# Kernel tuning notes

Hardware: AMD Instinct MI355X
Metric: run time of the kernel (lower is better)

Reference implementation:

```python
import jax, jax.numpy as jnp
import numpy as np

B, S, D, H = 2, 2048, 1024, 16
DK = D // H
SCALE = DK ** 0.5


def setup_inputs() -> dict:
    key = jax.random.key(0)
    ks = jax.random.split(key, 5)
    std = 1.0 / np.sqrt(D)
    return {
        "x": jax.random.normal(ks[0], (B, S, D), dtype=jnp.float32),
        "Wq": jax.random.normal(ks[1], (D, D), dtype=jnp.float32) * std,
        "Wk": jax.random.normal(ks[2], (D, D), dtype=jnp.float32) * std,
        "Wv": jax.random.normal(ks[3], (D, D), dtype=jnp.float32) * std,
        "Wo": jax.random.normal(ks[4], (D, D), dtype=jnp.float32) * std,
    }


def _split_heads(t):
    # [B, S, D] -> [B, H, S, DK]
    b, s, d = t.shape
    return t.reshape(b, s, H, DK).transpose(0, 2, 1, 3)


def reference(x, Wq, Wk, Wv, Wo):
    b, s, d = x.shape
    q = _split_heads(x @ Wq)
    k = _split_heads(x @ Wk)
    v = _split_heads(x @ Wv)
    # scores: [B, H, S, S]
    score = jnp.einsum("bhqd,bhkd->bhqk", q, k)
    causal = jnp.tril(jnp.ones((s, s), dtype=bool))[None, None]
    score = jnp.where(causal, score, -jnp.inf)
    attn = jax.nn.softmax(score / SCALE, axis=-1)
    out = jnp.einsum("bhqk,bhkd->bhqd", attn, v)
    out = out.transpose(0, 2, 1, 3).reshape(b, s, d)
    return out @ Wo
```

## Files before the change

### kernel.cpp

```cpp
#include <hip/hip_runtime.h>
#include <hip/hip_bf16.h>

typedef __bf16 bf16;
typedef __bf16 bf16x4 __attribute__((ext_vector_type(4)));
typedef __bf16 bf16x8 __attribute__((ext_vector_type(8)));
typedef float f32x4 __attribute__((ext_vector_type(4)));

#define MFMA16(a, b, c) __builtin_amdgcn_mfma_f32_16x16x32_bf16((a), (b), (c), 0, 0, 0)

__device__ __forceinline__ void async16(const void* g, void* l) {
  typedef const unsigned int __attribute__((address_space(1))) * GP;
  typedef unsigned int __attribute__((address_space(3))) * LP;
  __builtin_amdgcn_global_load_lds((GP)g, (LP)l, 16, 0, 0);
}

__global__ __launch_bounds__(256) void prep(
    const float* __restrict__ w0, const float* __restrict__ w1,
    const float* __restrict__ w2, const float* __restrict__ w3,
    const float* __restrict__ x, bf16* __restrict__ wtOut,
    bf16* __restrict__ xOut) {
  const int t = threadIdx.x;
  if (blockIdx.z == 4) {
    size_t base = ((size_t)(blockIdx.y * 16 + blockIdx.x)) * 16384;
#pragma unroll
    for (int p = 0; p < 16; ++p) {
      size_t i = base + (size_t)(p * 256 + t) * 4;
      f32x4 v = *(const f32x4*)&x[i];
      bf16 o[4];
#pragma unroll
      for (int j = 0; j < 4; ++j) o[j] = (bf16)v[j];
      *(ulong1*)&xOut[i] = *(ulong1*)o;
    }
    return;
  }
  __shared__ __align__(16) float tile[64][68];
  const float* src = (blockIdx.z == 0) ? w0 : (blockIdx.z == 1) ? w1
                   : (blockIdx.z == 2) ? w2 : w3;
  bf16* dst = wtOut + (size_t)blockIdx.z * (1024u * 1024u);
  const int bx = blockIdx.x, by = blockIdx.y;
#pragma unroll
  for (int p = 0; p < 4; ++p) {
    int idx = t + p * 256;
    int r = idx >> 4, c4 = idx & 15;
    *(f32x4*)&tile[r][c4 * 4] =
        *(const f32x4*)&src[(size_t)(by * 64 + r) * 1024 + bx * 64 + c4 * 4];
  }
  __syncthreads();
#pragma unroll
  for (int p = 0; p < 2; ++p) {
    int idx = t + p * 256;
    int rn = idx >> 3, c8 = idx & 7;
    bf16x8 v;
#pragma unroll
    for (int i = 0; i < 8; ++i) v[i] = (bf16)tile[c8 * 8 + i][rn];
    *(bf16x8*)&dst[(size_t)(bx * 64 + rn) * 1024 + by * 64 + c8 * 8] = v;
  }
}

template <typename OutT, int NI>
__global__ __launch_bounds__(256, 4) void gemm_bt(
    const bf16* __restrict__ A, const bf16* __restrict__ Bt,
    OutT* __restrict__ C, int btStrideZ, int cStrideZ, float scaleZ0,
    bf16* __restrict__ vtOut) {
  constexpr int XT = 1024 / (NI * 32);
  const int bid = blockIdx.x;
  const int rr = bid & 7, tt = bid >> 3;
  const int xb = tt % XT, yb = (tt / XT) * 8 + rr;
  const int zi = blockIdx.y;

  const int tid = threadIdx.x;
  const int wave = tid >> 6, lane = tid & 63;
  const int quad = lane >> 4, l16 = lane & 15;
  const int wm = wave >> 1, wn = wave & 1;
  const int m0 = yb * 128, n0 = xb * (NI * 32);
  const bf16* Bz = Bt + (size_t)zi * (size_t)btStrideZ;
  OutT* Cz = C + (size_t)zi * (size_t)cStrideZ;
  const float sc = (zi == 0) ? scaleZ0 : 1.0f;

  __shared__ __align__(16) bf16 lsA[2][128 * 32];
  __shared__ __align__(16) bf16 lsB[2][NI * 32 * 32];

  const int lrow = lane >> 2;
  const int cgX = (lane & 3) ^ ((lrow >> 1) & 3);
  const int fR = (l16 >> 1) & 3;

  f32x4 acc[4][NI];
#pragma unroll
  for (int i = 0; i < 4; ++i)
#pragma unroll
    for (int j = 0; j < NI; ++j) acc[i][j] = (f32x4){0.f, 0.f, 0.f, 0.f};

#pragma unroll
  for (int c = 0; c < 2; ++c) {
    int chunk = wave * 2 + c;
    int row = chunk * 16 + lrow;
    async16(&A[(size_t)(m0 + row) * 1024 + cgX * 8], &lsA[0][chunk * 512]);
  }
#pragma unroll
  for (int c = 0; c < NI / 2; ++c) {
    int chunk = wave * (NI / 2) + c;
    int row = chunk * 16 + lrow;
    async16(&Bz[(size_t)(n0 + row) * 1024 + cgX * 8], &lsB[0][chunk * 512]);
  }
  __syncthreads();

  for (int it = 0; it < 32; ++it) {
    const int cur = it & 1;
    if (it < 31) {
      int k0n = (it + 1) * 32;
#pragma unroll
      for (int c = 0; c < 2; ++c) {
        int chunk = wave * 2 + c;
        int row = chunk * 16 + lrow;
        async16(&A[(size_t)(m0 + row) * 1024 + k0n + cgX * 8],
                &lsA[cur ^ 1][chunk * 512]);
      }
#pragma unroll
      for (int c = 0; c < NI / 2; ++c) {
        int chunk = wave * (NI / 2) + c;
        int row = chunk * 16 + lrow;
        async16(&Bz[(size_t)(n0 + row) * 1024 + k0n + cgX * 8],
                &lsB[cur ^ 1][chunk * 512]);
      }
    }

    bf16x8 af[4], bfr[NI];
#pragma unroll
    for (int i = 0; i < 4; ++i) {
      int ra = wm * 64 + i * 16 + l16;
      af[i] = *(const bf16x8*)&lsA[cur][ra * 32 + ((quad ^ fR) * 8)];
    }
#pragma unroll
    for (int ni = 0; ni < NI; ++ni) {
      int rb = wn * (NI * 16) + ni * 16 + l16;
      bfr[ni] = *(const bf16x8*)&lsB[cur][rb * 32 + ((quad ^ fR) * 8)];
    }
#pragma unroll
    for (int mi = 0; mi < 4; ++mi)
#pragma unroll
      for (int ni = 0; ni < NI; ++ni)
        acc[mi][ni] = MFMA16(af[mi], bfr[ni], acc[mi][ni]);

    __syncthreads();
  }

  if (zi == 2 && vtOut != nullptr) {
#pragma unroll
    for (int mi = 0; mi < 4; ++mi)
#pragma unroll
      for (int ni = 0; ni < NI; ++ni) {
        int col = n0 + wn * (NI * 16) + ni * 16 + l16;
        int hd = col >> 6, d = col & 63;
        int row = m0 + wm * 64 + mi * 16 + quad * 4;
        int b = row >> 11, s = row & 2047;
        int s32 = s & 31;
        int sp = (s & ~31) + ((s32 & 12) << 1) + ((s32 >> 4) << 2);
        bf16 o[4];
#pragma unroll
        for (int r = 0; r < 4; ++r) o[r] = (bf16)acc[mi][ni][r];
        *(ulong1*)&vtOut[((size_t)(b * 16 + hd) * 64 + d) * 2048 + sp] =
            *(ulong1*)o;
      }
  } else {
#pragma unroll
    for (int mi = 0; mi < 4; ++mi)
#pragma unroll
      for (int ni = 0; ni < NI; ++ni) {
        int col = n0 + wn * (NI * 16) + ni * 16 + l16;
#pragma unroll
        for (int r = 0; r < 4; ++r) {
          int row = m0 + wm * 64 + mi * 16 + quad * 4 + r;
          Cz[(size_t)row * 1024 + col] = (OutT)(acc[mi][ni][r] * sc);
        }
      }
  }
}

__global__ __launch_bounds__(512, 4) void attn_fwd(
    const bf16* __restrict__ Q, const bf16* __restrict__ K,
    const bf16* __restrict__ Vt, bf16* __restrict__ O) {
  const int bid = blockIdx.x;
  const int x = bid & 15, hb = bid >> 4;
  const int h = hb & 15, b = hb >> 4;
  const int qt = b ? (15 - x) : x;
  const int tid = threadIdx.x;
  const int wave = tid >> 6, lane = tid & 63;
  const int quad = lane >> 4, l16 = lane & 15;
  const int wq = wave >> 1;
  const int par = wave & 1;

  __shared__ __align__(16) bf16 SMEM[32768];
  bf16* Qs = &SMEM[16384];

  const size_t base = ((size_t)b * 2048) * 1024 + (size_t)h * 64;
  const bf16* Qb = Q + base;
  const bf16* Kb = K + base;
  const bf16* Vtb = Vt + ((size_t)(b * 16 + h)) * 64 * 2048;
  bf16* Ob = O + base;

  const int lrow = lane >> 3;
  const int cgX = (lane & 7) ^ lrow;

#pragma unroll
  for (int c = 0; c < 2; ++c) {
    int chunk = wave * 2 + c;
    int row = chunk * 8 + lrow;
    async16(&Qb[(size_t)(qt * 128 + row) * 1024 + cgX * 8], &Qs[chunk * 512]);
  }
  {
    int row = wave * 8 + lrow;
    async16(&Kb[(size_t)row * 1024 + cgX * 8], &SMEM[0 * 8192 + wave * 512]);
    async16(&Vtb[(size_t)row * 2048 + cgX * 8],
            &SMEM[0 * 8192 + 4096 + wave * 512]);
    async16(&Kb[(size_t)(64 + row) * 1024 + cgX * 8],
            &SMEM[1 * 8192 + wave * 512]);
    async16(&Vtb[(size_t)row * 2048 + 64 + cgX * 8],
            &SMEM[1 * 8192 + 4096 + wave * 512]);
  }
  __syncthreads();

  bf16x8 aq[2][2];
#pragma unroll
  for (int g = 0; g < 2; ++g)
#pragma unroll
    for (int ks = 0; ks < 2; ++ks) {
      int row = wq * 32 + g * 16 + l16;
      aq[g][ks] =
          *(const bf16x8*)&Qs[row * 64 + (((ks * 4 + quad) ^ (l16 & 7)) * 8)];
    }
  __syncthreads();

  const float NEG_INF = -__builtin_inff();
  f32x4 lsv[2];
  f32x4 Oacc[2][4];
#pragma unroll
  for (int g = 0; g < 2; ++g) {
    lsv[g] = (f32x4){0.f, 0.f, 0.f, 0.f};
#pragma unroll
    for (int nt = 0; nt < 4; ++nt) Oacc[g][nt] = (f32x4){0.f, 0.f, 0.f, 0.f};
  }

  const int two_qt = 2 * qt;
  const int kt_end = 2 * qt + 1;

  for (int ktp = 0; ktp <= two_qt; ktp += 2) {
    {
      int row = wave * 8 + lrow;
      if (ktp + 2 <= kt_end) {
        int s2 = (ktp + 2) & 3;
        async16(&Kb[(size_t)((ktp + 2) * 64 + row) * 1024 + cgX * 8],
                &SMEM[s2 * 8192 + wave * 512]);
        async16(&Vtb[(size_t)row * 2048 + (ktp + 2) * 64 + cgX * 8],
                &SMEM[s2 * 8192 + 4096 + wave * 512]);
      }
      if (ktp + 3 <= kt_end) {
        int s3 = (ktp + 3) & 3;
        async16(&Kb[(size_t)((ktp + 3) * 64 + row) * 1024 + cgX * 8],
                &SMEM[s3 * 8192 + wave * 512]);
        async16(&Vtb[(size_t)row * 2048 + (ktp + 3) * 64 + cgX * 8],
                &SMEM[s3 * 8192 + 4096 + wave * 512]);
      }
    }

    const int kt = ktp + par;
    const int ko = (kt & 3) * 8192;
    const int vo = ko + 4096;
    const bool diag = (ktp == two_qt);
    const bool active = !diag || (par == 0) || (wq >= 2);

    if (active) {
#pragma unroll
      for (int a = 0; a < 2; ++a) {
        f32x4 s[2][2];
#pragma unroll
        for (int t = 0; t < 2; ++t) {
          const int nt = 2 * a + t;
          const int row = nt * 16 + l16;
          bf16x8 bk0 =
              *(const bf16x8*)&SMEM[ko + row * 64 + ((quad ^ (l16 & 7)) * 8)];
          bf16x8 bk1 = *(const bf16x8*)&SMEM[ko + row * 64 +
                                             (((4 + quad) ^ (l16 & 7)) * 8)];
#pragma unroll
          for (int g = 0; g < 2; ++g) {
            f32x4 sv = (f32x4){0.f, 0.f, 0.f, 0.f};
            sv = MFMA16(bk0, aq[g][0], sv);
            sv = MFMA16(bk1, aq[g][1], sv);
            s[g][t] = sv;
          }
        }

        if (diag) {
#pragma unroll
          for (int g = 0; g < 2; ++g) {
            const int q_rel = wq * 32 + g * 16 + l16;
#pragma unroll
            for (int t = 0; t < 2; ++t) {
              const int kb = par * 64 + (2 * a + t) * 16 + quad * 4;
#pragma unroll
              for (int r = 0; r < 4; ++r)
                if (kb + r > q_rel) s[g][t][r] = NEG_INF;
            }
          }
        }

        bf16x8 apf[2];
#pragma unroll
        for (int g = 0; g < 2; ++g) {
#pragma unroll
          for (int t = 0; t < 2; ++t) {
#pragma unroll
            for (int r = 0; r < 4; ++r) s[g][t][r] = exp2f(s[g][t][r]);
            lsv[g] += s[g][t];
          }
          bf16x4 c0 = __builtin_convertvector(s[g][0], bf16x4);
          bf16x4 c1 = __builtin_convertvector(s[g][1], bf16x4);
#pragma unroll
          for (int i = 0; i < 4; ++i) {
            apf[g][i] = c0[i];
            apf[g][4 + i] = c1[i];
          }
        }

#pragma unroll
        for (int nt = 0; nt < 4; ++nt) {
          const int R = nt * 16 + l16;
          bf16x8 bvf = *(const bf16x8*)&SMEM[vo + R * 64 +
                                             (((a * 4 + quad) ^ (l16 & 7)) *
                                              8)];
#pragma unroll
          for (int g = 0; g < 2; ++g)
            Oacc[g][nt] = MFMA16(apf[g], bvf, Oacc[g][nt]);
        }
      }
    }

    __syncthreads();
  }

  float ls[2];
#pragma unroll
  for (int g = 0; g < 2; ++g) {
    float a_ = lsv[g][0] + lsv[g][1] + lsv[g][2] + lsv[g][3];
    a_ += __shfl_xor(a_, 16, 64);
    a_ += __shfl_xor(a_, 32, 64);
    ls[g] = a_;
  }

  float* F = (float*)SMEM;
  const int roff = wq * 2176;
  if (par == 1) {
#pragma unroll
    for (int g = 0; g < 2; ++g) {
#pragma unroll
      for (int nt = 0; nt < 4; ++nt)
        *(f32x4*)&F[roff + (g * 4 + nt) * 256 + lane * 4] = Oacc[g][nt];
      F[roff + 2048 + g * 64 + lane] = ls[g];
    }
  }
  __syncthreads();
  if (par == 0) {
#pragma unroll
    for (int g = 0; g < 2; ++g) {
#pragma unroll
      for (int nt = 0; nt < 4; ++nt)
        Oacc[g][nt] += *(const f32x4*)&F[roff + (g * 4 + nt) * 256 + lane * 4];
      ls[g] += F[roff + 2048 + g * 64 + lane];
    }
    float rl[2][4];
#pragma unroll
    for (int g = 0; g < 2; ++g)
#pragma unroll
      for (int r = 0; r < 4; ++r)
        rl[g][r] = 1.f / __shfl(ls[g], quad * 4 + r, 64);
#pragma unroll
    for (int g = 0; g < 2; ++g)
#pragma unroll
      for (int nt = 0; nt < 4; ++nt)
#pragma unroll
        for (int r = 0; r < 4; ++r) {
          int row = qt * 128 + wq * 32 + g * 16 + quad * 4 + r;
          Ob[(size_t)row * 1024 + nt * 16 + l16] =
              (bf16)(Oacc[g][nt][r] * rl[g][r]);
        }
  }
}

extern "C" void kernel_launch(void* const* d_in, const int* in_sizes, int n_in,
                              void* d_out, int out_size, void* d_ws,
                              size_t ws_size, hipStream_t stream) {
  (void)in_sizes; (void)n_in; (void)out_size; (void)ws_size;
  const float* x  = (const float*)d_in[0];
  const float* Wq = (const float*)d_in[1];
  const float* Wk = (const float*)d_in[2];
  const float* Wv = (const float*)d_in[3];
  const float* Wo = (const float*)d_in[4];
  float* out = (float*)d_out;

  bf16* ws = (bf16*)d_ws;
  const size_t WELEM = 1024u * 1024u;
  const size_t TELEM = 4096u * 1024u;
  bf16* wt  = ws;
  bf16* xbf = ws + 4 * WELEM;
  bf16* q   = xbf + TELEM;
  bf16* k   = q + TELEM;
  bf16* vt  = k + TELEM;
  bf16* ao  = vt + TELEM;

  const float QSCALE = 0.125f * 1.44269504088896340736f;

  prep<<<dim3(16, 16, 5), 256, 0, stream>>>(Wq, Wk, Wv, Wo, x, wt, xbf);
  gemm_bt<bf16, 4><<<dim3(256, 3), 256, 0, stream>>>(
      xbf, wt, q, (int)WELEM, (int)TELEM, QSCALE, vt);
  attn_fwd<<<dim3(512), 512, 0, stream>>>(q, k, vt, ao);
  gemm_bt<float, 2><<<dim3(512, 1), 256, 0, stream>>>(
      ao, wt + 3 * WELEM, out, 0, 0, 1.0f, nullptr);
}
```

Measured before the change: 169.6 us.

## Add 256x256-tile QKV projection GEMM kernel with 512 threads

Replaces the generic QKV projection GEMM with a dedicated kernel using 256x256 output tiles, 8 waves, double-buffered async global-to-LDS loads with XOR swizzle, and setprio around the MFMA bursts. Larger tiles raise arithmetic intensity and cut redundant global loads of A and B. In exchange the grid shrinks to 192 blocks on a 256-CU device, and the 128 KB of LDS plus 128 accumulator floats per lane may limit occupancy. The output stores are scalar bf16 writes instead of vectorized ones.

Result: slower. 173.1 us (+2.1%).

```diff
diff --git a/kernel.cpp b/kernel.cpp
--- a/kernel.cpp
+++ b/kernel.cpp
@@ -54,6 +54,132 @@
 #pragma unroll
     for (int i = 0; i < 8; ++i) v[i] = (bf16)tile[c8 * 8 + i][rn];
     *(bf16x8*)&dst[(size_t)(bx * 64 + rn) * 1024 + by * 64 + c8 * 8] = v;
+  }
+}
+
+__global__ __launch_bounds__(512, 2) void qkv256(
+    const bf16* __restrict__ A, const bf16* __restrict__ Bt,
+    bf16* __restrict__ C, int btStrideZ, int cStrideZ, float scaleZ0,
+    bf16* __restrict__ vtOut) {
+  const int bid = blockIdx.x;
+  const int rr = bid & 7, tt = bid >> 3;
+  const int xb = tt & 3, yb = (tt >> 2) * 8 + rr;
+  const int zi = blockIdx.y;
+
+  const int tid = threadIdx.x;
+  const int wave = tid >> 6, lane = tid & 63;
+  const int quad = lane >> 4, l16 = lane & 15;
+  const int wm = wave >> 2, wn = wave & 3;
+  const int m0 = yb * 256, n0 = xb * 256;
+  const bf16* Bz = Bt + (size_t)zi * (size_t)btStrideZ;
+  bf16* Cz = C + (size_t)zi * (size_t)cStrideZ;
+  const float sc = (zi == 0) ? scaleZ0 : 1.0f;
+
+  __shared__ __align__(16) bf16 lsA[2][256 * 64];
+  __shared__ __align__(16) bf16 lsB[2][256 * 64];
+
+  const int lrow = lane >> 3;
+  const int cgX = (lane & 7) ^ lrow;
+
+  f32x4 acc[8][4];
+#pragma unroll
+  for (int i = 0; i < 8; ++i)
+#pragma unroll
+    for (int j = 0; j < 4; ++j) acc[i][j] = (f32x4){0.f, 0.f, 0.f, 0.f};
+
+#define QKV_STAGE(buf, kt)                                                   \
+  {                                                                          \
+    const int k0_ = (kt)*64;                                                 \
+    _Pragma("unroll") for (int c = 0; c < 4; ++c) {                          \
+      int chunk = wave * 4 + c;                                              \
+      int row = chunk * 8 + lrow;                                            \
+      async16(&A[(size_t)(m0 + row) * 1024 + k0_ + cgX * 8],                 \
+              &lsA[buf][chunk * 512]);                                       \
+    }                                                                        \
+    _Pragma("unroll") for (int c = 0; c < 4; ++c) {                          \
+      int chunk = wave * 4 + c;                                              \
+      int row = chunk * 8 + lrow;                                            \
+      async16(&Bz[(size_t)(n0 + row) * 1024 + k0_ + cgX * 8],                \
+              &lsB[buf][chunk * 512]);                                       \
+    }                                                                        \
+  }
+
+  QKV_STAGE(0, 0);
+  QKV_STAGE(1, 1);
+  asm volatile("s_waitcnt vmcnt(8)" ::: "memory");
+  __builtin_amdgcn_s_barrier();
+
+  for (int kt = 0; kt < 16; ++kt) {
+    const int cur = kt & 1;
+#pragma unroll
+    for (int ks = 0; ks < 2; ++ks) {
+      bf16x8 bfr[4];
+#pragma unroll
+      for (int ni = 0; ni < 4; ++ni) {
+        int rb = wn * 64 + ni * 16 + l16;
+        bfr[ni] = *(const bf16x8*)&lsB[cur][rb * 64 +
+                                            (((ks * 4 + quad) ^ (l16 & 7)) *
+                                             8)];
+      }
+#pragma unroll
+      for (int mh = 0; mh < 2; ++mh) {
+        bf16x8 af[4];
+#pragma unroll
+        for (int i = 0; i < 4; ++i) {
+          int ra = wm * 128 + (mh * 4 + i) * 16 + l16;
+          af[i] = *(const bf16x8*)&lsA[cur][ra * 64 +
+                                            (((ks * 4 + quad) ^ (l16 & 7)) *
+                                             8)];
+        }
+        __builtin_amdgcn_s_setprio(1);
+#pragma unroll
+        for (int i = 0; i < 4; ++i)
+#pragma unroll
+          for (int ni = 0; ni < 4; ++ni)
+            acc[mh * 4 + i][ni] = MFMA16(af[i], bfr[ni], acc[mh * 4 + i][ni]);
+        __builtin_amdgcn_s_setprio(0);
+      }
+    }
+    __builtin_amdgcn_s_barrier();
+    if (kt + 2 < 16) {
+      QKV_STAGE(cur, kt + 2);
+      asm volatile("s_waitcnt vmcnt(8)" ::: "memory");
+    } else {
+      asm volatile("s_waitcnt vmcnt(0)" ::: "memory");
+    }
+    __builtin_amdgcn_s_barrier();
+  }
+#undef QKV_STAGE
+
+  if (zi == 2 && vtOut != nullptr) {
+#pragma unroll
+    for (int mi = 0; mi < 8; ++mi)
+#pragma unroll
+      for (int ni = 0; ni < 4; ++ni) {
+        int col = n0 + wn * 64 + ni * 16 + l16;
+        int hd = col >> 6, d = col & 63;
+        int row = m0 + wm * 128 + mi * 16 + quad * 4;
+        int b = row >> 11, s = row & 2047;
+        int s32 = s & 31;
+        int sp = (s & ~31) + ((s32 & 12) << 1) + ((s32 >> 4) << 2);
+        bf16 o[4];
+#pragma unroll
+        for (int r = 0; r < 4; ++r) o[r] = (bf16)acc[mi][ni][r];
+        *(ulong1*)&vtOut[((size_t)(b * 16 + hd) * 64 + d) * 2048 + sp] =
+            *(ulong1*)o;
+      }
+  } else {
+#pragma unroll
+    for (int mi = 0; mi < 8; ++mi)
+#pragma unroll
+      for (int ni = 0; ni < 4; ++ni) {
+        int col = n0 + wn * 64 + ni * 16 + l16;
+#pragma unroll
+        for (int r = 0; r < 4; ++r) {
+          int row = m0 + wm * 128 + mi * 16 + quad * 4 + r;
+          Cz[(size_t)row * 1024 + col] = (bf16)(acc[mi][ni][r] * sc);
+        }
+      }
   }
 }
 
@@ -409,7 +535,7 @@
   const float QSCALE = 0.125f * 1.44269504088896340736f;
 
   prep<<<dim3(16, 16, 5), 256, 0, stream>>>(Wq, Wk, Wv, Wo, x, wt, xbf);
-  gemm_bt<bf16, 4><<<dim3(256, 3), 256, 0, stream>>>(
+  qkv256<<<dim3(64, 3), 512, 0, stream>>>(
       xbf, wt, q, (int)WELEM, (int)TELEM, QSCALE, vt);
   attn_fwd<<<dim3(512), 512, 0, stream>>>(q, k, vt, ao);
   gemm_bt<float, 2><<<dim3(512, 1), 256, 0, stream>>>(
```

## Restructure attention to 4 waves with per-wave KV loop and XCD-aware block mapping

Applied to the files above, without the earlier changes.

The attention kernel moves from 8 waves, where pairs split the key tiles by parity and merge through shared memory, to 4 waves that each walk every key tile, with a double buffer instead of a 4-stage ring. This drops the cross-wave reduction, one barrier and some LDS, and block indices are remapped so each XCD handles a fixed set of batch-heads for L2 locality. It also adds s_setprio around the MFMAs and uses the raw hardware exp2. The trade-off is fewer waves per block and less prefetch depth, which may expose load latency.

Result: no change. 167.3 us (-1.3%).

```diff
diff --git a/kernel.cpp b/kernel.cpp
--- a/kernel.cpp
+++ b/kernel.cpp
@@ -176,20 +176,22 @@
   }
 }
 
-__global__ __launch_bounds__(512, 4) void attn_fwd(
+__global__ __launch_bounds__(256, 3) void attn_fwd(
     const bf16* __restrict__ Q, const bf16* __restrict__ K,
     const bf16* __restrict__ Vt, bf16* __restrict__ O) {
   const int bid = blockIdx.x;
-  const int x = bid & 15, hb = bid >> 4;
-  const int h = hb & 15, b = hb >> 4;
-  const int qt = b ? (15 - x) : x;
+  const int xcd = bid & 7;
+  const int i = bid >> 3;
+  const int g4 = i & 3;
+  const int j = i >> 2;
+  const int qt = (j < 8) ? j : (23 - j);
+  const int bh = xcd * 4 + g4;
+  const int h = bh & 15, b = bh >> 4;
   const int tid = threadIdx.x;
   const int wave = tid >> 6, lane = tid & 63;
   const int quad = lane >> 4, l16 = lane & 15;
-  const int wq = wave >> 1;
-  const int par = wave & 1;
-
-  __shared__ __align__(16) bf16 SMEM[32768];
+
+  __shared__ __align__(16) bf16 SMEM[24576];
   bf16* Qs = &SMEM[16384];
 
   const size_t base = ((size_t)b * 2048) * 1024 + (size_t)h * 64;
@@ -202,20 +204,17 @@
   const int cgX = (lane & 7) ^ lrow;
 
 #pragma unroll
+  for (int c = 0; c < 4; ++c) {
+    int chunk = wave * 4 + c;
+    int row = chunk * 8 + lrow;
+    async16(&Qb[(size_t)(qt * 128 + row) * 1024 + cgX * 8], &Qs[chunk * 512]);
+  }
+#pragma unroll
   for (int c = 0; c < 2; ++c) {
     int chunk = wave * 2 + c;
     int row = chunk * 8 + lrow;
-    async16(&Qb[(size_t)(qt * 128 + row) * 1024 + cgX * 8], &Qs[chunk * 512]);
-  }
-  {
-    int row = wave * 8 + lrow;
-    async16(&Kb[(size_t)row * 1024 + cgX * 8], &SMEM[0 * 8192 + wave * 512]);
-    async16(&Vtb[(size_t)row * 2048 + cgX * 8],
-            &SMEM[0 * 8192 + 4096 + wave * 512]);
-    async16(&Kb[(size_t)(64 + row) * 1024 + cgX * 8],
-            &SMEM[1 * 8192 + wave * 512]);
-    async16(&Vtb[(size_t)row * 2048 + 64 + cgX * 8],
-            &SMEM[1 * 8192 + 4096 + wave * 512]);
+    async16(&Kb[(size_t)row * 1024 + cgX * 8], &SMEM[chunk * 512]);
+    async16(&Vtb[(size_t)row * 2048 + cgX * 8], &SMEM[4096 + chunk * 512]);
   }
   __syncthreads();
 
@@ -224,11 +223,10 @@
   for (int g = 0; g < 2; ++g)
 #pragma unroll
     for (int ks = 0; ks < 2; ++ks) {
-      int row = wq * 32 + g * 16 + l16;
+      int row = wave * 32 + g * 16 + l16;
       aq[g][ks] =
           *(const bf16x8*)&Qs[row * 64 + (((ks * 4 + quad) ^ (l16 & 7)) * 8)];
     }
-  __syncthreads();
 
   const float NEG_INF = -__builtin_inff();
   f32x4 lsv[2];
@@ -240,35 +238,30 @@
     for (int nt = 0; nt < 4; ++nt) Oacc[g][nt] = (f32x4){0.f, 0.f, 0.f, 0.f};
   }
 
-  const int two_qt = 2 * qt;
-  const int kt_end = 2 * qt + 1;
-
-  for (int ktp = 0; ktp <= two_qt; ktp += 2) {
-    {
-      int row = wave * 8 + lrow;
-      if (ktp + 2 <= kt_end) {
-        int s2 = (ktp + 2) & 3;
-        async16(&Kb[(size_t)((ktp + 2) * 64 + row) * 1024 + cgX * 8],
-                &SMEM[s2 * 8192 + wave * 512]);
-        async16(&Vtb[(size_t)row * 2048 + (ktp + 2) * 64 + cgX * 8],
-                &SMEM[s2 * 8192 + 4096 + wave * 512]);
-      }
-      if (ktp + 3 <= kt_end) {
-        int s3 = (ktp + 3) & 3;
-        async16(&Kb[(size_t)((ktp + 3) * 64 + row) * 1024 + cgX * 8],
-                &SMEM[s3 * 8192 + wave * 512]);
-        async16(&Vtb[(size_t)row * 2048 + (ktp + 3) * 64 + cgX * 8],
-                &SMEM[s3 * 8192 + 4096 + wave * 512]);
-      }
-    }
-
-    const int kt = ktp + par;
-    const int ko = (kt & 3) * 8192;
+  const int ktmax = 2 * qt + 1;
+  const int ktd = 2 * qt + (wave >> 1);
+
+  for (int kt = 0; kt <= ktmax; ++kt) {
+    const int cur = kt & 1;
+    if (kt < ktmax) {
+      const int ns = (cur ^ 1) * 8192;
+#pragma unroll
+      for (int c = 0; c < 2; ++c) {
+        int chunk = wave * 2 + c;
+        int row = chunk * 8 + lrow;
+        async16(&Kb[(size_t)((kt + 1) * 64 + row) * 1024 + cgX * 8],
+                &SMEM[ns + chunk * 512]);
+        async16(&Vtb[(size_t)row * 2048 + (kt + 1) * 64 + cgX * 8],
+                &SMEM[ns + 4096 + chunk * 512]);
+      }
+    }
+
+    const int ko = cur * 8192;
     const int vo = ko + 4096;
-    const bool diag = (ktp == two_qt);
-    const bool active = !diag || (par == 0) || (wq >= 2);
-
-    if (active) {
+
+    if (kt <= ktd) {
+      const int cb = (kt - 2 * qt) * 64;
+      const bool diag = (kt == ktd);
 #pragma unroll
       for (int a = 0; a < 2; ++a) {
         f32x4 s[2][2];
@@ -280,6 +273,7 @@
               *(const bf16x8*)&SMEM[ko + row * 64 + ((quad ^ (l16 & 7)) * 8)];
           bf16x8 bk1 = *(const bf16x8*)&SMEM[ko + row * 64 +
                                              (((4 + quad) ^ (l16 & 7)) * 8)];
+          __builtin_amdgcn_s_setprio(1);
 #pragma unroll
           for (int g = 0; g < 2; ++g) {
             f32x4 sv = (f32x4){0.f, 0.f, 0.f, 0.f};
@@ -287,15 +281,16 @@
             sv = MFMA16(bk1, aq[g][1], sv);
             s[g][t] = sv;
           }
+          __builtin_amdgcn_s_setprio(0);
         }
 
         if (diag) {
 #pragma unroll
           for (int g = 0; g < 2; ++g) {
-            const int q_rel = wq * 32 + g * 16 + l16;
+            const int q_rel = wave * 32 + g * 16 + l16;
 #pragma unroll
             for (int t = 0; t < 2; ++t) {
-              const int kb = par * 64 + (2 * a + t) * 16 + quad * 4;
+              const int kb = cb + (2 * a + t) * 16 + quad * 4;
 #pragma unroll
               for (int r = 0; r < 4; ++r)
                 if (kb + r > q_rel) s[g][t][r] = NEG_INF;
@@ -309,15 +304,16 @@
 #pragma unroll
           for (int t = 0; t < 2; ++t) {
 #pragma unroll
-            for (int r = 0; r < 4; ++r) s[g][t][r] = exp2f(s[g][t][r]);
+            for (int r = 0; r < 4; ++r)
+              s[g][t][r] = __builtin_amdgcn_exp2f(s[g][t][r]);
             lsv[g] += s[g][t];
           }
           bf16x4 c0 = __builtin_convertvector(s[g][0], bf16x4);
           bf16x4 c1 = __builtin_convertvector(s[g][1], bf16x4);
 #pragma unroll
-          for (int i = 0; i < 4; ++i) {
-            apf[g][i] = c0[i];
-            apf[g][4 + i] = c1[i];
+          for (int i2 = 0; i2 < 4; ++i2) {
+            apf[g][i2] = c0[i2];
+            apf[g][4 + i2] = c1[i2];
           }
         }
 
@@ -327,9 +323,11 @@
           bf16x8 bvf = *(const bf16x8*)&SMEM[vo + R * 64 +
                                              (((a * 4 + quad) ^ (l16 & 7)) *
                                               8)];
+          __builtin_amdgcn_s_setprio(1);
 #pragma unroll
           for (int g = 0; g < 2; ++g)
             Oacc[g][nt] = MFMA16(apf[g], bvf, Oacc[g][nt]);
+          __builtin_amdgcn_s_setprio(0);
         }
       }
     }
@@ -345,44 +343,22 @@
     a_ += __shfl_xor(a_, 32, 64);
     ls[g] = a_;
   }
-
-  float* F = (float*)SMEM;
-  const int roff = wq * 2176;
-  if (par == 1) {
-#pragma unroll
-    for (int g = 0; g < 2; ++g) {
-#pragma unroll
-      for (int nt = 0; nt < 4; ++nt)
-        *(f32x4*)&F[roff + (g * 4 + nt) * 256 + lane * 4] = Oacc[g][nt];
-      F[roff + 2048 + g * 64 + lane] = ls[g];
-    }
-  }
-  __syncthreads();
-  if (par == 0) {
-#pragma unroll
-    for (int g = 0; g < 2; ++g) {
-#pragma unroll
-      for (int nt = 0; nt < 4; ++nt)
-        Oacc[g][nt] += *(const f32x4*)&F[roff + (g * 4 + nt) * 256 + lane * 4];
-      ls[g] += F[roff + 2048 + g * 64 + lane];
-    }
-    float rl[2][4];
-#pragma unroll
-    for (int g = 0; g < 2; ++g)
-#pragma unroll
-      for (int r = 0; r < 4; ++r)
-        rl[g][r] = 1.f / __shfl(ls[g], quad * 4 + r, 64);
-#pragma unroll
-    for (int g = 0; g < 2; ++g)
-#pragma unroll
-      for (int nt = 0; nt < 4; ++nt)
-#pragma unroll
-        for (int r = 0; r < 4; ++r) {
-          int row = qt * 128 + wq * 32 + g * 16 + quad * 4 + r;
-          Ob[(size_t)row * 1024 + nt * 16 + l16] =
-              (bf16)(Oacc[g][nt][r] * rl[g][r]);
-        }
-  }
+  float rl[2][4];
+#pragma unroll
+  for (int g = 0; g < 2; ++g)
+#pragma unroll
+    for (int r = 0; r < 4; ++r)
+      rl[g][r] = 1.f / __shfl(ls[g], quad * 4 + r, 64);
+#pragma unroll
+  for (int g = 0; g < 2; ++g)
+#pragma unroll
+    for (int nt = 0; nt < 4; ++nt)
+#pragma unroll
+      for (int r = 0; r < 4; ++r) {
+        int row = qt * 128 + wave * 32 + g * 16 + quad * 4 + r;
+        Ob[(size_t)row * 1024 + nt * 16 + l16] =
+            (bf16)(Oacc[g][nt][r] * rl[g][r]);
+      }
 }
 
 extern "C" void kernel_launch(void* const* d_in, const int* in_sizes, int n_in,
@@ -411,7 +387,7 @@
   prep<<<dim3(16, 16, 5), 256, 0, stream>>>(Wq, Wk, Wv, Wo, x, wt, xbf);
   gemm_bt<bf16, 4><<<dim3(256, 3), 256, 0, stream>>>(
       xbf, wt, q, (int)WELEM, (int)TELEM, QSCALE, vt);
-  attn_fwd<<<dim3(512), 512, 0, stream>>>(q, k, vt, ao);
+  attn_fwd<<<dim3(512), 256, 0, stream>>>(q, k, vt, ao);
   gemm_bt<float, 2><<<dim3(512, 1), 256, 0, stream>>>(
       ao, wt + 3 * WELEM, out, 0, 0, 1.0f, nullptr);
 }
```
